# Performance work log

Hardware: AMD Instinct MI355X
Metric: run time of the kernel (lower is better)

## Reference

```python
import jax, jax.numpy as jnp
import numpy as np

B, F, H, T = 2048, 128, 512, 96  # batch, n_features, hidden_size, output_length


def setup_inputs() -> dict:
    key = jax.random.key(0)
    ks = jax.random.split(key, 7)
    s_ih = 1.0 / np.sqrt(H)
    return {
        "hidden": jax.random.normal(ks[0], (B, H), dtype=jnp.float32),
        "w_ih": jax.random.uniform(ks[1], (3 * H, F), jnp.float32, -s_ih, s_ih),
        "w_hh": jax.random.uniform(ks[2], (3 * H, H), jnp.float32, -s_ih, s_ih),
        "b_ih": jax.random.uniform(ks[3], (3 * H,), jnp.float32, -s_ih, s_ih),
        "b_hh": jax.random.uniform(ks[4], (3 * H,), jnp.float32, -s_ih, s_ih),
        "fc_w": jax.random.uniform(ks[5], (F, H), jnp.float32, -s_ih, s_ih),
        "fc_b": jax.random.uniform(ks[6], (F,), jnp.float32, -s_ih, s_ih),
    }


def reference(hidden, w_ih, w_hh, b_ih, b_hh, fc_w, fc_b):
    x0 = jnp.zeros((hidden.shape[0], F), dtype=hidden.dtype)  # initial_input=None

    def step(carry, _):
        h, x = carry
        gi = x @ w_ih.T + b_ih            # [B, 3H]
        gh = h @ w_hh.T + b_hh            # [B, 3H]
        i_r, i_z, i_n = jnp.split(gi, 3, axis=-1)
        h_r, h_z, h_n = jnp.split(gh, 3, axis=-1)
        r = jax.nn.sigmoid(i_r + h_r)
        z = jax.nn.sigmoid(i_z + h_z)
        n = jnp.tanh(i_n + r * h_n)
        h_new = (1.0 - z) * n + z * h
        x_new = h_new @ fc_w.T + fc_b     # [B, F]
        return (h_new, x_new), x_new

    _, ys = jax.lax.scan(step, (hidden, x0), None, length=T)  # [T, B, F]
    out = jnp.transpose(ys, (1, 0, 2))     # [B, T, F]
    out = out[:, ::-1, :]                  # backwards=True: outputs.insert(0, ...)
    return out
```

## Files before the change

kernel.cpp:

```cpp
#include <hip/hip_runtime.h>
#include <hip/hip_bf16.h>

#define HH 512
#define FF 128
#define BB 2048
#define TT 96
#define NSTEP 96
#define NGATE 2048
#define NTOT 2176
#define GRP 16
#define CPB 32

typedef short short8 __attribute__((ext_vector_type(8)));
typedef float f32x4 __attribute__((ext_vector_type(4)));

__device__ __forceinline__ float sigmoidf_(float x) { return 1.f / (1.f + __expf(-x)); }
__device__ __forceinline__ float tanhf_(float x) {
    float e = __expf(-2.f * fabsf(x));
    float t = (1.f - e) / (1.f + e);
    return x < 0.f ? -t : t;
}

__device__ __forceinline__ size_t frag_off(int m, int k, int K) {
    return (size_t)((m >> 4) * (K >> 5) + (k >> 5)) * 1024
         + (size_t)(((k >> 3) & 3) * 256 + (m & 15) * 16 + (k & 7) * 2);
}

__device__ __forceinline__ short bf16bits(float f) {
    __hip_bfloat16 b = __float2bfloat16(f);
    return *(short*)&b;
}

__global__ __launch_bounds__(256) void build_weights(
    const float* __restrict__ w_ih, const float* __restrict__ w_hh,
    const float* __restrict__ b_ih, const float* __restrict__ b_hh,
    const float* __restrict__ fc_w, const float* __restrict__ fc_b,
    char* __restrict__ Wg, char* __restrict__ W0g, char* __restrict__ Wfc,
    float* __restrict__ bias, float* __restrict__ bias0)
{
    const int n = blockIdx.x;
    const int tid = threadIdx.x;
    __shared__ float wih_s[FF];
    const bool is_out = (n >= NGATE);
    int gate = 3, gidx = 0, f = 0;
    if (is_out) {
        f = n - NGATE;
    } else {
        int j = (n >> 4) * 4 + ((n >> 2) & 3);
        gate = n & 3;
        gidx = (gate == 0) ? j : (gate == 1) ? (512 + j) : (1024 + j);
    }
    if (!is_out && gate != 3 && tid < FF) wih_s[tid] = w_ih[gidx * FF + tid];
    __syncthreads();

    for (int k = tid; k < HH; k += 256) {
        float w, w0;
        if (is_out) {
            w = fc_w[f * HH + k];
            w0 = 0.f;
        } else if (gate == 3) {
            w = w_hh[gidx * HH + k];
            w0 = w;
        } else {
            float comb = 0.f;
#pragma unroll 8
            for (int ff2 = 0; ff2 < FF; ++ff2) comb += wih_s[ff2] * fc_w[ff2 * HH + k];
            if (gate == 2) { w = comb; w0 = 0.f; }
            else { float whh = w_hh[gidx * HH + k]; w = whh + comb; w0 = whh; }
        }
        if (is_out) {
            *(short*)(Wfc + frag_off(f, k, HH)) = bf16bits(w);
        } else {
            *(short*)(Wg  + frag_off(n, k, HH)) = bf16bits(w);
            *(short*)(W0g + frag_off(n, k, HH)) = bf16bits(w0);
        }
    }
    if (tid == 0 && !is_out) {
        float b, b0;
        float cb = 0.f;
        if (gate != 3)
            for (int ff2 = 0; ff2 < FF; ++ff2) cb += fc_b[ff2] * w_ih[gidx * FF + ff2];
        if (gate <= 1)      { float s2 = b_ih[gidx] + b_hh[gidx]; b = s2 + cb; b0 = s2; }
        else if (gate == 2) { b = b_ih[gidx] + cb; b0 = b_ih[gidx]; }
        else                { b = b_hh[gidx]; b0 = b_hh[gidx]; }
        bias[n] = b; bias0[n] = b0;
    }
}

__global__ __launch_bounds__(256) void init_misc(
    const float* __restrict__ hidden, char* __restrict__ hfrag, int* __restrict__ cnt)
{
    int i = blockIdx.x * 256 + threadIdx.x;
    int row = i >> 6, k0 = (i & 63) << 3;
    short8 v;
#pragma unroll
    for (int t = 0; t < 8; ++t) v[t] = bf16bits(hidden[(size_t)row * HH + k0 + t]);
    *(short8*)(hfrag + frag_off(row, k0, HH)) = v;
    if (i < GRP * NSTEP * CPB) cnt[i] = 0;
}

__global__ __launch_bounds__(256, 2) void gru_persist(
    const char* __restrict__ Wg, const char* __restrict__ W0g, const char* __restrict__ Wfc,
    const float* __restrict__ bias, const float* __restrict__ bias0,
    const float* __restrict__ fc_b, const float* __restrict__ hidden,
    char* __restrict__ hfrag0, char* __restrict__ hfrag1,
    float* __restrict__ out, int* __restrict__ cnt)
{
    __shared__ __align__(16) short Bs[32768];
    __shared__ __align__(16) short hfr[2048];

    const int tid = threadIdx.x;
    const int lane = tid & 63, w = tid >> 6;
    const int l15 = lane & 15, quad = lane >> 4;
    const int g = blockIdx.x & 15, c = blockIdx.x >> 4;

    const int jtb = (w >> 1) * 2;
    const int rbase = (w & 1) * 64;
    const int cbase = jtb * 4;

    const char* aB0 = hfrag0 + (size_t)(g * 8 + (w & 1) * 4) * 16384 + lane * 16;
    const char* aB1 = hfrag1 + (size_t)(g * 8 + (w & 1) * 4) * 16384 + lane * 16;
    const char* bf  = Wfc + (size_t)(c & 7) * 16384 + lane * 16;
    const char* wlds = (const char*)Bs + (size_t)jtb * 16384 + lane * 16;
    const bool fcsel = (w == 0) || (w == 3);
    const int fcq = c >> 3;

    f32x4 bv4[2];
#pragma unroll
    for (int jtl = 0; jtl < 2; ++jtl)
        bv4[jtl] = *(const f32x4*)&bias[(c * 4 + jtb + jtl) * 16 + quad * 4];
    const f32x4 fcb4 = *(const f32x4*)&fc_b[(c & 7) * 16 + quad * 4];

    float carry[2][4];
#pragma unroll
    for (int jtl = 0; jtl < 2; ++jtl)
#pragma unroll
        for (int bt = 0; bt < 4; ++bt)
            carry[jtl][bt] =
                hidden[(size_t)(g * 128 + rbase + bt * 16 + l15) * HH
                       + c * 16 + cbase + jtl * 4 + quad];

    int* const fl = cnt + g * (NSTEP * CPB);

    {
        const char* wsrc = Wg + (size_t)c * 65536;
#pragma unroll
        for (int i = 0; i < 16; ++i) {
            int idx = i * 256 + tid;
            *(int4*)((char*)Bs + idx * 16) = *(const int4*)(wsrc + (size_t)idx * 16);
        }
    }
    __syncthreads();

    auto grp_wait = [&](int s) {
        if (w == 0) {
            if (lane < 32) {
                const int* fp = fl + s * CPB + lane;
                while (__hip_atomic_load(fp, __ATOMIC_RELAXED, __HIP_MEMORY_SCOPE_AGENT) == 0)
                    __builtin_amdgcn_s_sleep(1);
            }
            asm volatile("buffer_inv sc0\n\ts_waitcnt vmcnt(0)" ::: "memory");
        }
        __syncthreads();
        asm volatile("" ::: "memory");
    };

    auto epilogue = [&](f32x4 (&acc)[2][4], int s, char* hout) {
#pragma unroll
        for (int jtl = 0; jtl < 2; ++jtl)
#pragma unroll
            for (int bt = 0; bt < 4; ++bt) {
                f32x4 a = acc[jtl][bt];
                float r  = sigmoidf_(a[0]);
                float z  = sigmoidf_(a[1]);
                float nv = tanhf_(a[2] + r * a[3]);
                float hn = (1.f - z) * nv + z * carry[jtl][bt];
                carry[jtl][bt] = hn;
                hfr[(rbase + bt * 16 + l15) * 16 + cbase + jtl * 4 + quad] = bf16bits(hn);
            }
        __syncthreads();
        {
            int lrow = tid >> 1, half = tid & 1;
            size_t off = (size_t)((g * 8 + (lrow >> 4)) * 16 + (c >> 1)) * 1024
                       + (size_t)((((c << 1) + half) & 3) * 256 + (lrow & 15) * 16);
            *(int4*)(hout + off) = *(const int4*)&hfr[lrow * 16 + half * 8];
        }
        asm volatile("s_waitcnt vmcnt(0)" ::: "memory");
        __syncthreads();
        if (tid == 0)
            __hip_atomic_store(fl + s * CPB + c, 1, __ATOMIC_RELAXED, __HIP_MEMORY_SCOPE_AGENT);
    };

    {
        f32x4 acc[2][4];
#pragma unroll
        for (int jtl = 0; jtl < 2; ++jtl) {
            f32x4 b0 = *(const f32x4*)&bias0[(c * 4 + jtb + jtl) * 16 + quad * 4];
#pragma unroll
            for (int bt = 0; bt < 4; ++bt) acc[jtl][bt] = b0;
        }
        const char* w0b = W0g + (size_t)(c * 4 + jtb) * 16384 + lane * 16;
        short8 W0[2][2]; short8 Hb[2][4];
#pragma unroll
        for (int p = 0; p < 2; ++p) {
#pragma unroll
            for (int jtl = 0; jtl < 2; ++jtl)
                W0[p][jtl] = *(const short8*)(w0b + (jtl * 16 + p) * 1024);
#pragma unroll
            for (int bt = 0; bt < 4; ++bt)
                Hb[p][bt] = *(const short8*)(aB0 + bt * 16384 + p * 1024);
        }
#pragma unroll
        for (int it = 0; it < 16; ++it) {
            const int sl = it & 1;
#pragma unroll
            for (int jtl = 0; jtl < 2; ++jtl)
#pragma unroll
                for (int bt = 0; bt < 4; ++bt)
                    acc[jtl][bt] = __builtin_amdgcn_mfma_f32_16x16x32_bf16(W0[sl][jtl], Hb[sl][bt], acc[jtl][bt], 0, 0, 0);
            if (it + 2 < 16) {
#pragma unroll
                for (int jtl = 0; jtl < 2; ++jtl)
                    W0[sl][jtl] = *(const short8*)(w0b + (jtl * 16 + it + 2) * 1024);
#pragma unroll
                for (int bt = 0; bt < 4; ++bt)
                    Hb[sl][bt] = *(const short8*)(aB0 + bt * 16384 + (it + 2) * 1024);
            }
        }
        epilogue(acc, 0, hfrag1);
    }

    for (int s = 1; s < 96; ++s) {
        const char* ab = (s & 1) ? aB1 : aB0;
        char* hout = (s & 1) ? hfrag0 : hfrag1;
        const bool dofc = fcsel && ((s & 3) == fcq);

        f32x4 acc[2][4];
#pragma unroll
        for (int jtl = 0; jtl < 2; ++jtl)
#pragma unroll
            for (int bt = 0; bt < 4; ++bt) acc[jtl][bt] = bv4[jtl];
        f32x4 fca[4] = {{0.f,0.f,0.f,0.f},{0.f,0.f,0.f,0.f},{0.f,0.f,0.f,0.f},{0.f,0.f,0.f,0.f}};

        short8 Wa[2][2]; short8 Wf[2];
#pragma unroll
        for (int p = 0; p < 2; ++p)
#pragma unroll
            for (int jtl = 0; jtl < 2; ++jtl)
                Wa[p][jtl] = *(const short8*)(wlds + (size_t)(jtl * 16 + p) * 1024);
        if (dofc) {
            Wf[0] = *(const short8*)(bf);
            Wf[1] = *(const short8*)(bf + 1024);
        }

        grp_wait(s - 1);

        short8 Hb[4][4];
#pragma unroll
        for (int p = 0; p < 4; ++p)
#pragma unroll
            for (int bt = 0; bt < 4; ++bt)
                Hb[p][bt] = *(const short8*)(ab + bt * 16384 + p * 1024);

#pragma unroll
        for (int it = 0; it < 16; ++it) {
            const int sa = it & 3, sw = it & 1;
#pragma unroll
            for (int jtl = 0; jtl < 2; ++jtl)
#pragma unroll
                for (int bt = 0; bt < 4; ++bt)
                    acc[jtl][bt] = __builtin_amdgcn_mfma_f32_16x16x32_bf16(Wa[sw][jtl], Hb[sa][bt], acc[jtl][bt], 0, 0, 0);
            if (dofc) {
#pragma unroll
                for (int bt = 0; bt < 4; ++bt)
                    fca[bt] = __builtin_amdgcn_mfma_f32_16x16x32_bf16(Wf[sw], Hb[sa][bt], fca[bt], 0, 0, 0);
            }
            if (it + 4 < 16) {
#pragma unroll
                for (int bt = 0; bt < 4; ++bt)
                    Hb[sa][bt] = *(const short8*)(ab + bt * 16384 + (it + 4) * 1024);
            }
            if (it + 2 < 16) {
#pragma unroll
                for (int jtl = 0; jtl < 2; ++jtl)
                    Wa[sw][jtl] = *(const short8*)(wlds + (size_t)(jtl * 16 + it + 2) * 1024);
                if (dofc) Wf[sw] = *(const short8*)(bf + (size_t)(it + 2) * 1024);
            }
        }

        if (dofc) {
            const int tt = 96 - s;
#pragma unroll
            for (int bt = 0; bt < 4; ++bt) {
                f32x4 v = fca[bt] + fcb4;
                *(f32x4*)&out[(size_t)(g * 128 + rbase + bt * 16 + l15) * (TT * FF)
                              + tt * FF + (c & 7) * 16 + quad * 4] = v;
            }
        }

        epilogue(acc, s, hout);
    }

    grp_wait(95);
    if (fcsel && fcq == 0) {
        f32x4 fca[4] = {{0.f,0.f,0.f,0.f},{0.f,0.f,0.f,0.f},{0.f,0.f,0.f,0.f},{0.f,0.f,0.f,0.f}};
        short8 Wf[2]; short8 Hb[2][4];
#pragma unroll
        for (int p = 0; p < 2; ++p) {
            Wf[p] = *(const short8*)(bf + (size_t)p * 1024);
#pragma unroll
            for (int bt = 0; bt < 4; ++bt)
                Hb[p][bt] = *(const short8*)(aB0 + bt * 16384 + p * 1024);
        }
#pragma unroll
        for (int it = 0; it < 16; ++it) {
            const int sl = it & 1;
#pragma unroll
            for (int bt = 0; bt < 4; ++bt)
                fca[bt] = __builtin_amdgcn_mfma_f32_16x16x32_bf16(Wf[sl], Hb[sl][bt], fca[bt], 0, 0, 0);
            if (it + 2 < 16) {
                Wf[sl] = *(const short8*)(bf + (size_t)(it + 2) * 1024);
#pragma unroll
                for (int bt = 0; bt < 4; ++bt)
                    Hb[sl][bt] = *(const short8*)(aB0 + bt * 16384 + (it + 2) * 1024);
            }
        }
#pragma unroll
        for (int bt = 0; bt < 4; ++bt) {
            f32x4 v = fca[bt] + fcb4;
            *(f32x4*)&out[(size_t)(g * 128 + rbase + bt * 16 + l15) * (TT * FF)
                          + (c & 7) * 16 + quad * 4] = v;
        }
    }
}

extern "C" void kernel_launch(void* const* d_in, const int* in_sizes, int n_in,
                              void* d_out, int out_size, void* d_ws, size_t ws_size,
                              hipStream_t stream) {
    const float* hidden = (const float*)d_in[0];
    const float* w_ih   = (const float*)d_in[1];
    const float* w_hh   = (const float*)d_in[2];
    const float* b_ih   = (const float*)d_in[3];
    const float* b_hh   = (const float*)d_in[4];
    const float* fc_w   = (const float*)d_in[5];
    const float* fc_b   = (const float*)d_in[6];
    float* out = (float*)d_out;

    char* ws = (char*)d_ws;
    size_t off = 0;
    auto alloc = [&](size_t bytes) -> void* {
        void* p = ws + off;
        off += (bytes + 255) & ~(size_t)255;
        return p;
    };
    char* Wg   = (char*)alloc((size_t)NGATE * HH * 2);
    char* W0g  = (char*)alloc((size_t)NGATE * HH * 2);
    char* Wfc  = (char*)alloc((size_t)FF * HH * 2);
    float* bias  = (float*)alloc(NGATE * 4);
    float* bias0 = (float*)alloc(NGATE * 4);
    char* hfrag0 = (char*)alloc((size_t)BB * HH * 2);
    char* hfrag1 = (char*)alloc((size_t)BB * HH * 2);
    int* cnt = (int*)alloc((size_t)GRP * NSTEP * CPB * 4);

    build_weights<<<NTOT, 256, 0, stream>>>(w_ih, w_hh, b_ih, b_hh, fc_w, fc_b,
                                            Wg, W0g, Wfc, bias, bias0);
    init_misc<<<(BB * HH / 8 + 255) / 256, 256, 0, stream>>>(hidden, hfrag0, cnt);
    gru_persist<<<512, 256, 0, stream>>>(Wg, W0g, Wfc, bias, bias0, fc_b, hidden,
                                         hfrag0, hfrag1, out, cnt);
}
```

Baseline: 959.9 us.

## Repartition warp tiles to cover all gate columns and split batch rows

Each warp now computes all four gate-column tiles of the block for 32 batch rows, replacing the old 2 column tiles by 64 rows split. Every warp therefore reads the full LDS weight slice but only two global h-fragment tiles, and the h prefetch depth grows from 4 to 6 stages. The FC projection is now spread across all four warps, each doing two tiles, instead of two warps doing four. This trades more LDS weight traffic and register pressure for less global h traffic per warp and a balanced FC load.

```diff
diff --git a/kernel.cpp b/kernel.cpp
--- a/kernel.cpp
+++ b/kernel.cpp
@@ -114,31 +114,26 @@
     const int l15 = lane & 15, quad = lane >> 4;
     const int g = blockIdx.x & 15, c = blockIdx.x >> 4;
 
-    const int jtb = (w >> 1) * 2;
-    const int rbase = (w & 1) * 64;
-    const int cbase = jtb * 4;
-
-    const char* aB0 = hfrag0 + (size_t)(g * 8 + (w & 1) * 4) * 16384 + lane * 16;
-    const char* aB1 = hfrag1 + (size_t)(g * 8 + (w & 1) * 4) * 16384 + lane * 16;
+    const char* aB0 = hfrag0 + (size_t)(g * 8 + w * 2) * 16384 + lane * 16;
+    const char* aB1 = hfrag1 + (size_t)(g * 8 + w * 2) * 16384 + lane * 16;
     const char* bf  = Wfc + (size_t)(c & 7) * 16384 + lane * 16;
-    const char* wlds = (const char*)Bs + (size_t)jtb * 16384 + lane * 16;
-    const bool fcsel = (w == 0) || (w == 3);
+    const char* wlds = (const char*)Bs + lane * 16;
     const int fcq = c >> 3;
 
-    f32x4 bv4[2];
-#pragma unroll
-    for (int jtl = 0; jtl < 2; ++jtl)
-        bv4[jtl] = *(const f32x4*)&bias[(c * 4 + jtb + jtl) * 16 + quad * 4];
+    f32x4 bv4[4];
+#pragma unroll
+    for (int mt = 0; mt < 4; ++mt)
+        bv4[mt] = *(const f32x4*)&bias[c * 64 + mt * 16 + quad * 4];
     const f32x4 fcb4 = *(const f32x4*)&fc_b[(c & 7) * 16 + quad * 4];
 
-    float carry[2][4];
-#pragma unroll
-    for (int jtl = 0; jtl < 2; ++jtl)
-#pragma unroll
-        for (int bt = 0; bt < 4; ++bt)
-            carry[jtl][bt] =
-                hidden[(size_t)(g * 128 + rbase + bt * 16 + l15) * HH
-                       + c * 16 + cbase + jtl * 4 + quad];
+    float carry[4][2];
+#pragma unroll
+    for (int mt = 0; mt < 4; ++mt)
+#pragma unroll
+        for (int btl = 0; btl < 2; ++btl)
+            carry[mt][btl] =
+                hidden[(size_t)(g * 128 + w * 32 + btl * 16 + l15) * HH
+                       + c * 16 + mt * 4 + quad];
 
     int* const fl = cnt + g * (NSTEP * CPB);
 
@@ -165,18 +160,18 @@
         asm volatile("" ::: "memory");
     };
 
-    auto epilogue = [&](f32x4 (&acc)[2][4], int s, char* hout) {
-#pragma unroll
-        for (int jtl = 0; jtl < 2; ++jtl)
-#pragma unroll
-            for (int bt = 0; bt < 4; ++bt) {
-                f32x4 a = acc[jtl][bt];
+    auto epilogue = [&](f32x4 (&acc)[4][2], int s, char* hout) {
+#pragma unroll
+        for (int mt = 0; mt < 4; ++mt)
+#pragma unroll
+            for (int btl = 0; btl < 2; ++btl) {
+                f32x4 a = acc[mt][btl];
                 float r  = sigmoidf_(a[0]);
                 float z  = sigmoidf_(a[1]);
                 float nv = tanhf_(a[2] + r * a[3]);
-                float hn = (1.f - z) * nv + z * carry[jtl][bt];
-                carry[jtl][bt] = hn;
-                hfr[(rbase + bt * 16 + l15) * 16 + cbase + jtl * 4 + quad] = bf16bits(hn);
+                float hn = (1.f - z) * nv + z * carry[mt][btl];
+                carry[mt][btl] = hn;
+                hfr[(w * 32 + btl * 16 + l15) * 16 + mt * 4 + quad] = bf16bits(hn);
             }
         __syncthreads();
         {
@@ -192,39 +187,38 @@
     };
 
     {
-        f32x4 acc[2][4];
-#pragma unroll
-        for (int jtl = 0; jtl < 2; ++jtl) {
-            f32x4 b0 = *(const f32x4*)&bias0[(c * 4 + jtb + jtl) * 16 + quad * 4];
-#pragma unroll
-            for (int bt = 0; bt < 4; ++bt) acc[jtl][bt] = b0;
-        }
-        const char* w0b = W0g + (size_t)(c * 4 + jtb) * 16384 + lane * 16;
-        short8 W0[2][2]; short8 Hb[2][4];
+        f32x4 acc[4][2];
+#pragma unroll
+        for (int mt = 0; mt < 4; ++mt) {
+            f32x4 b0 = *(const f32x4*)&bias0[c * 64 + mt * 16 + quad * 4];
+            acc[mt][0] = b0; acc[mt][1] = b0;
+        }
+        const char* w0b = W0g + (size_t)c * 65536 + lane * 16;
+        short8 W0[2][4]; short8 Hb[2][2];
 #pragma unroll
         for (int p = 0; p < 2; ++p) {
 #pragma unroll
-            for (int jtl = 0; jtl < 2; ++jtl)
-                W0[p][jtl] = *(const short8*)(w0b + (jtl * 16 + p) * 1024);
-#pragma unroll
-            for (int bt = 0; bt < 4; ++bt)
-                Hb[p][bt] = *(const short8*)(aB0 + bt * 16384 + p * 1024);
+            for (int mt = 0; mt < 4; ++mt)
+                W0[p][mt] = *(const short8*)(w0b + (size_t)(mt * 16 + p) * 1024);
+#pragma unroll
+            for (int btl = 0; btl < 2; ++btl)
+                Hb[p][btl] = *(const short8*)(aB0 + btl * 16384 + p * 1024);
         }
 #pragma unroll
         for (int it = 0; it < 16; ++it) {
             const int sl = it & 1;
 #pragma unroll
-            for (int jtl = 0; jtl < 2; ++jtl)
-#pragma unroll
-                for (int bt = 0; bt < 4; ++bt)
-                    acc[jtl][bt] = __builtin_amdgcn_mfma_f32_16x16x32_bf16(W0[sl][jtl], Hb[sl][bt], acc[jtl][bt], 0, 0, 0);
+            for (int mt = 0; mt < 4; ++mt)
+#pragma unroll
+                for (int btl = 0; btl < 2; ++btl)
+                    acc[mt][btl] = __builtin_amdgcn_mfma_f32_16x16x32_bf16(W0[sl][mt], Hb[sl][btl], acc[mt][btl], 0, 0, 0);
             if (it + 2 < 16) {
 #pragma unroll
-                for (int jtl = 0; jtl < 2; ++jtl)
-                    W0[sl][jtl] = *(const short8*)(w0b + (jtl * 16 + it + 2) * 1024);
-#pragma unroll
-                for (int bt = 0; bt < 4; ++bt)
-                    Hb[sl][bt] = *(const short8*)(aB0 + bt * 16384 + (it + 2) * 1024);
+                for (int mt = 0; mt < 4; ++mt)
+                    W0[sl][mt] = *(const short8*)(w0b + (size_t)(mt * 16 + it + 2) * 1024);
+#pragma unroll
+                for (int btl = 0; btl < 2; ++btl)
+                    Hb[sl][btl] = *(const short8*)(aB0 + btl * 16384 + (it + 2) * 1024);
             }
         }
         epilogue(acc, 0, hfrag1);
@@ -233,21 +227,21 @@
     for (int s = 1; s < 96; ++s) {
         const char* ab = (s & 1) ? aB1 : aB0;
         char* hout = (s & 1) ? hfrag0 : hfrag1;
-        const bool dofc = fcsel && ((s & 3) == fcq);
-
-        f32x4 acc[2][4];
-#pragma unroll
-        for (int jtl = 0; jtl < 2; ++jtl)
-#pragma unroll
-            for (int bt = 0; bt < 4; ++bt) acc[jtl][bt] = bv4[jtl];
-        f32x4 fca[4] = {{0.f,0.f,0.f,0.f},{0.f,0.f,0.f,0.f},{0.f,0.f,0.f,0.f},{0.f,0.f,0.f,0.f}};
-
-        short8 Wa[2][2]; short8 Wf[2];
+        const bool dofc = ((s & 3) == fcq);
+
+        f32x4 acc[4][2];
+#pragma unroll
+        for (int mt = 0; mt < 4; ++mt) {
+            acc[mt][0] = bv4[mt]; acc[mt][1] = bv4[mt];
+        }
+        f32x4 fca[2] = {{0.f,0.f,0.f,0.f},{0.f,0.f,0.f,0.f}};
+
+        short8 Wa[2][4]; short8 Wf[2];
 #pragma unroll
         for (int p = 0; p < 2; ++p)
 #pragma unroll
-            for (int jtl = 0; jtl < 2; ++jtl)
-                Wa[p][jtl] = *(const short8*)(wlds + (size_t)(jtl * 16 + p) * 1024);
+            for (int mt = 0; mt < 4; ++mt)
+                Wa[p][mt] = *(const short8*)(wlds + (size_t)(mt * 16 + p) * 1024);
         if (dofc) {
             Wf[0] = *(const short8*)(bf);
             Wf[1] = *(const short8*)(bf + 1024);
@@ -255,35 +249,34 @@
 
         grp_wait(s - 1);
 
-        short8 Hb[4][4];
-#pragma unroll
-        for (int p = 0; p < 4; ++p)
-#pragma unroll
-            for (int bt = 0; bt < 4; ++bt)
-                Hb[p][bt] = *(const short8*)(ab + bt * 16384 + p * 1024);
+        short8 Hb[6][2];
+#pragma unroll
+        for (int p = 0; p < 6; ++p)
+#pragma unroll
+            for (int btl = 0; btl < 2; ++btl)
+                Hb[p][btl] = *(const short8*)(ab + btl * 16384 + p * 1024);
 
 #pragma unroll
         for (int it = 0; it < 16; ++it) {
-            const int sa = it & 3, sw = it & 1;
-#pragma unroll
-            for (int jtl = 0; jtl < 2; ++jtl)
-#pragma unroll
-                for (int bt = 0; bt < 4; ++bt)
-                    acc[jtl][bt] = __builtin_amdgcn_mfma_f32_16x16x32_bf16(Wa[sw][jtl], Hb[sa][bt], acc[jtl][bt], 0, 0, 0);
+            const int sa = it % 6, sw = it & 1;
+#pragma unroll
+            for (int mt = 0; mt < 4; ++mt)
+#pragma unroll
+                for (int btl = 0; btl < 2; ++btl)
+                    acc[mt][btl] = __builtin_amdgcn_mfma_f32_16x16x32_bf16(Wa[sw][mt], Hb[sa][btl], acc[mt][btl], 0, 0, 0);
             if (dofc) {
-#pragma unroll
-                for (int bt = 0; bt < 4; ++bt)
-                    fca[bt] = __builtin_amdgcn_mfma_f32_16x16x32_bf16(Wf[sw], Hb[sa][bt], fca[bt], 0, 0, 0);
-            }
-            if (it + 4 < 16) {
-#pragma unroll
-                for (int bt = 0; bt < 4; ++bt)
-                    Hb[sa][bt] = *(const short8*)(ab + bt * 16384 + (it + 4) * 1024);
+                fca[0] = __builtin_amdgcn_mfma_f32_16x16x32_bf16(Wf[sw], Hb[sa][0], fca[0], 0, 0, 0);
+                fca[1] = __builtin_amdgcn_mfma_f32_16x16x32_bf16(Wf[sw], Hb[sa][1], fca[1], 0, 0, 0);
+            }
+            if (it + 6 < 16) {
+#pragma unroll
+                for (int btl = 0; btl < 2; ++btl)
+                    Hb[sa][btl] = *(const short8*)(ab + btl * 16384 + (it + 6) * 1024);
             }
             if (it + 2 < 16) {
 #pragma unroll
-                for (int jtl = 0; jtl < 2; ++jtl)
-                    Wa[sw][jtl] = *(const short8*)(wlds + (size_t)(jtl * 16 + it + 2) * 1024);
+                for (int mt = 0; mt < 4; ++mt)
+                    Wa[sw][mt] = *(const short8*)(wlds + (size_t)(mt * 16 + it + 2) * 1024);
                 if (dofc) Wf[sw] = *(const short8*)(bf + (size_t)(it + 2) * 1024);
             }
         }
@@ -291,9 +284,9 @@
         if (dofc) {
             const int tt = 96 - s;
 #pragma unroll
-            for (int bt = 0; bt < 4; ++bt) {
-                f32x4 v = fca[bt] + fcb4;
-                *(f32x4*)&out[(size_t)(g * 128 + rbase + bt * 16 + l15) * (TT * FF)
+            for (int btl = 0; btl < 2; ++btl) {
+                f32x4 v = fca[btl] + fcb4;
+                *(f32x4*)&out[(size_t)(g * 128 + w * 32 + btl * 16 + l15) * (TT * FF)
                               + tt * FF + (c & 7) * 16 + quad * 4] = v;
             }
         }
@@ -301,34 +294,33 @@
         epilogue(acc, s, hout);
     }
 
-    grp_wait(95);
-    if (fcsel && fcq == 0) {
-        f32x4 fca[4] = {{0.f,0.f,0.f,0.f},{0.f,0.f,0.f,0.f},{0.f,0.f,0.f,0.f},{0.f,0.f,0.f,0.f}};
-        short8 Wf[2]; short8 Hb[2][4];
+    if (fcq == 0) {
+        grp_wait(95);
+        f32x4 fca[2] = {{0.f,0.f,0.f,0.f},{0.f,0.f,0.f,0.f}};
+        short8 Wf[2]; short8 Hb[2][2];
 #pragma unroll
         for (int p = 0; p < 2; ++p) {
             Wf[p] = *(const short8*)(bf + (size_t)p * 1024);
 #pragma unroll
-            for (int bt = 0; bt < 4; ++bt)
-                Hb[p][bt] = *(const short8*)(aB0 + bt * 16384 + p * 1024);
+            for (int btl = 0; btl < 2; ++btl)
+                Hb[p][btl] = *(const short8*)(aB0 + btl * 16384 + p * 1024);
         }
 #pragma unroll
         for (int it = 0; it < 16; ++it) {
             const int sl = it & 1;
-#pragma unroll
-            for (int bt = 0; bt < 4; ++bt)
-                fca[bt] = __builtin_amdgcn_mfma_f32_16x16x32_bf16(Wf[sl], Hb[sl][bt], fca[bt], 0, 0, 0);
+            fca[0] = __builtin_amdgcn_mfma_f32_16x16x32_bf16(Wf[sl], Hb[sl][0], fca[0], 0, 0, 0);
+            fca[1] = __builtin_amdgcn_mfma_f32_16x16x32_bf16(Wf[sl], Hb[sl][1], fca[1], 0, 0, 0);
             if (it + 2 < 16) {
                 Wf[sl] = *(const short8*)(bf + (size_t)(it + 2) * 1024);
 #pragma unroll
-                for (int bt = 0; bt < 4; ++bt)
-                    Hb[sl][bt] = *(const short8*)(aB0 + bt * 16384 + (it + 2) * 1024);
-            }
-        }
-#pragma unroll
-        for (int bt = 0; bt < 4; ++bt) {
-            f32x4 v = fca[bt] + fcb4;
-            *(f32x4*)&out[(size_t)(g * 128 + rbase + bt * 16 + l15) * (TT * FF)
+                for (int btl = 0; btl < 2; ++btl)
+                    Hb[sl][btl] = *(const short8*)(aB0 + btl * 16384 + (it + 2) * 1024);
+            }
+        }
+#pragma unroll
+        for (int btl = 0; btl < 2; ++btl) {
+            f32x4 v = fca[btl] + fcb4;
+            *(f32x4*)&out[(size_t)(g * 128 + w * 32 + btl * 16 + l15) * (TT * FF)
                           + (c & 7) * 16 + quad * 4] = v;
         }
     }
```

New measurement: 809.6 us (median of 2 runs). 15.7% less time.
